# Performance work log

Measured on AMD Instinct MI355X. Metric: run time of the kernel, lower is better.

The kernel has to match this reference:

```python
import jax, jax.numpy as jnp
import numpy as np

KERNEL_BANDWIDTH = 0.3
STEP_SIZE = 0.5
NB_ITERATIONS = 4


def setup_inputs() -> dict:
    key = jax.random.key(0)
    # B x D x H x W pixel embeddings
    x_in = jax.random.normal(key, (2, 64, 96, 96), dtype=jnp.float32)
    return {"x_in": x_in}


def reference(x_in):
    B, D, H, W = x_in.shape
    N = H * W
    x0 = x_in.reshape(B, D, N)

    def body(x, _):
        # Gaussian-like kernel K[i,j] = exp(bw * <x_i, x_j>), symmetric NxN per batch
        K = jnp.exp(KERNEL_BANDWIDTH * jnp.einsum('bdn,bdm->bnm', x, x))  # (B,N,N)
        # torch: diag(K^T @ 1) then inverse of that diagonal == 1/column-sums
        colsum = jnp.sum(K, axis=1)  # (B,N)
        # x @ (K diag(1/colsum)): column-normalized weighted mean of embeddings
        xk = jnp.einsum('bdn,bnm->bdm', x, K) / colsum[:, None, :]
        x_new = STEP_SIZE * xk + (1.0 - STEP_SIZE) * x
        return x_new, x_new

    _, ys = jax.lax.scan(body, x0, None, length=NB_ITERATIONS)  # (I,B,D,N)
    allx = jnp.concatenate([x0[None], ys], axis=0)  # (I+1,B,D,N)
    # B x (I+1) x D x H x W
    return jnp.transpose(allx, (1, 0, 2, 3)).reshape(B, NB_ITERATIONS + 1, D, H, W)
```

## Files before the change

### kernel.cpp

```cpp
#include <hip/hip_runtime.h>
#include <hip/hip_bf16.h>

constexpr int B_    = 2;
constexpr int D_    = 64;
constexpr int N_    = 9216;
constexpr int ITERS = 4;

constexpr int MTQ     = 128;
constexpr int MBF     = N_ / MTQ;
constexpr int KS      = 4;
constexpr int KEYS_WG = N_ / KS;
constexpr int KTILES  = KEYS_WG / 128;
constexpr int NWG     = B_ * MBF * KS;
constexpr int PB      = 144;

constexpr float KBW  = 0.3f;
constexpr float STEP = 0.5f;
constexpr float C2   = 0.43280851226668905f;

using short8   = __attribute__((ext_vector_type(8))) short;
using float16v = __attribute__((ext_vector_type(16))) float;
typedef __attribute__((ext_vector_type(2))) __bf16 bf16x2;

__device__ __forceinline__ unsigned short f2bf(float f) {
  union { float f; unsigned u; } v; v.f = f;
  unsigned u = v.u;
  unsigned r = (u + 0x7fffu + ((u >> 16) & 1u)) >> 16;
  return (unsigned short)r;
}

#if __has_builtin(__builtin_amdgcn_cvt_pk_bf16_f32)
__device__ __forceinline__ unsigned pk2bf(float a, float b) {
  bf16x2 r = __builtin_amdgcn_cvt_pk_bf16_f32(a, b);
  union { bf16x2 h; unsigned u; } v; v.h = r; return v.u;
}
#else
__device__ __forceinline__ unsigned pk2bf(float a, float b) {
  return (unsigned)f2bf(a) | ((unsigned)f2bf(b) << 16);
}
#endif

__device__ __forceinline__ float csum2(unsigned u, float cs) {
#if __has_builtin(__builtin_amdgcn_fdot2_f32_bf16)
  union { unsigned x; bf16x2 h; } a, o;
  a.x = u; o.x = 0x3f803f80u;
  return __builtin_amdgcn_fdot2_f32_bf16(a.h, o.h, cs, false);
#else
  union { unsigned u; float f; } lo, hi;
  lo.u = u << 16; hi.u = u & 0xffff0000u;
  return cs + lo.f + hi.f;
#endif
}

__device__ __forceinline__ void dma16(const unsigned short* g,
                                      unsigned short* lds_base, int lane) {
#if __has_builtin(__builtin_amdgcn_global_load_lds)
  __builtin_amdgcn_global_load_lds(
      (const __attribute__((address_space(1))) unsigned int*)g,
      (__attribute__((address_space(3))) unsigned int*)lds_base, 16, 0, 0);
#else
  *(int4*)((char*)lds_base + lane * 16) = *(const int4*)g;
#endif
}

__global__ void prep_kernel(const float* __restrict__ xin, float* __restrict__ out,
                            unsigned short* __restrict__ XT,
                            unsigned short* __restrict__ Xbf)
{
  const int bx = blockIdx.x;
  const int nb = bx % PB, b = bx / PB;
  const int n0 = nb * 64;
  const int tid = threadIdx.x;
  __shared__ float tile[64 * 65];

  #pragma unroll
  for (int r = 0; r < 16; ++r) {
    int idx = r * 256 + tid;
    int d = idx >> 6, j = idx & 63;
    float v = xin[((size_t)b * 64 + d) * N_ + n0 + j];
    out[(((size_t)b * 5 + 0) * 64 + d) * N_ + n0 + j] = v;
    Xbf[((size_t)b * 64 + d) * N_ + n0 + j] = f2bf(v);
    tile[d * 65 + j] = v;
  }
  __syncthreads();
  #pragma unroll
  for (int r = 0; r < 16; ++r) {
    int idx = r * 256 + tid;
    int nl = idx >> 6, d = idx & 63;
    XT[((size_t)b * N_ + n0 + nl) * 64 + d] = f2bf(tile[d * 65 + nl]);
  }
}

__global__ void __launch_bounds__(256, 3) flash_kernel(
    const unsigned short* __restrict__ XT,
    const unsigned short* __restrict__ Xbf,
    float* __restrict__ pacc, float* __restrict__ pcs)
{
  const int bx   = blockIdx.x;
  const int ks   = bx & 3;
  const int mb   = (bx >> 2) % MBF;
  const int b    = bx / (MBF * KS);
  const int tid  = threadIdx.x;
  const int wave = tid >> 6, lane = tid & 63;
  const int c = lane & 31, h = lane >> 5;
  const int cp = (c & 0x13) | ((c & 4) << 1) | ((c & 8) >> 1);
  const int m0 = mb * MTQ;
  const int bpaddr = (lane ^ 32) << 2;

  const unsigned short* XTb = XT  + (size_t)b * N_ * 64;
  const unsigned short* Xb  = Xbf + (size_t)b * 64 * N_;

  __shared__ unsigned short sXT[128 * 64];
  __shared__ unsigned short sXB[64 * 128];

  short8 qf[4];
  #pragma unroll
  for (int k = 0; k < 4; ++k) {
    short8 raw = *(const short8*)(XTb +
        (size_t)(m0 + wave * 32 + c) * 64 + k * 16 + h * 8);
    unsigned o[4];
    const unsigned* rw = (const unsigned*)&raw;
    #pragma unroll
    for (int p4 = 0; p4 < 4; ++p4) {
      union { unsigned u; float f; } lo, hi;
      lo.u = rw[p4] << 16; hi.u = rw[p4] & 0xffff0000u;
      o[p4] = pk2bf(lo.f * C2, hi.f * C2);
    }
    qf[k] = *(const short8*)o;
  }

  float16v zv;
  #pragma unroll
  for (int p = 0; p < 16; ++p) zv[p] = 0.f;
  float16v acc[2];
  acc[0] = zv; acc[1] = zv;
  float cs = 0.f;

  const int xt_rr = lane >> 3, xt_sc = lane & 7;
  const int xb_rr = lane >> 4, xb_sc = lane & 15;

  int n0g = ks * KEYS_WG;
  for (int t = 0; t < KTILES; ++t, n0g += 128) {
    __syncthreads();
    #pragma unroll
    for (int ii = 0; ii < 4; ++ii) {
      int row = wave * 32 + ii * 8 + xt_rr;
      int gc  = xt_sc ^ (row & 7);
      dma16(XTb + (size_t)(n0g + row) * 64 + gc * 8,
            sXT + (wave * 32 + ii * 8) * 64, lane);
    }
    #pragma unroll
    for (int ii = 0; ii < 4; ++ii) {
      int row = wave * 16 + ii * 4 + xb_rr;
      int gc  = xb_sc ^ (row & 7);
      dma16(Xb + (size_t)row * N_ + n0g + gc * 8,
            sXB + (wave * 16 + ii * 4) * 128, lane);
    }
    __syncthreads();

    #pragma unroll
    for (int s = 0; s < 4; ++s) {
      short8 af[4];
      #pragma unroll
      for (int k = 0; k < 4; ++k)
        af[k] = *(const short8*)(sXT + (s * 32 + cp) * 64 +
                                 ((k * 2 + h) ^ (cp & 7)) * 8);

      float16v S = zv;
      #pragma unroll
      for (int k = 0; k < 4; ++k)
        S = __builtin_amdgcn_mfma_f32_32x32x16_bf16(af[k], qf[k], S, 0, 0, 0);

      unsigned q[8];
      #pragma unroll
      for (int g = 0; g < 8; ++g) {
        float w0 = __builtin_amdgcn_exp2f(S[2 * g]);
        float w1 = __builtin_amdgcn_exp2f(S[2 * g + 1]);
        unsigned u = pk2bf(w0, w1);
        q[g] = u;
        cs = csum2(u, cs);
      }

      union { unsigned d[4]; short8 s; } a20, a21;
      a20.d[0] = q[0]; a20.d[1] = q[1]; a20.d[2] = q[2]; a20.d[3] = q[3];
      a21.d[0] = q[4]; a21.d[1] = q[5]; a21.d[2] = q[6]; a21.d[3] = q[7];

      short8 b20[2], b21[2];
      #pragma unroll
      for (int dt = 0; dt < 2; ++dt) {
        b20[dt] = *(const short8*)(sXB + (dt * 32 + c) * 128 + ((4 * s + h)     ^ (c & 7)) * 8);
        b21[dt] = *(const short8*)(sXB + (dt * 32 + c) * 128 + ((4 * s + 2 + h) ^ (c & 7)) * 8);
      }
      #pragma unroll
      for (int dt = 0; dt < 2; ++dt)
        acc[dt] = __builtin_amdgcn_mfma_f32_32x32x16_bf16(a20.s, b20[dt], acc[dt], 0, 0, 0);
      #pragma unroll
      for (int dt = 0; dt < 2; ++dt)
        acc[dt] = __builtin_amdgcn_mfma_f32_32x32x16_bf16(a21.s, b21[dt], acc[dt], 0, 0, 0);
    }
  }

  union { float f; int i; } cu; cu.f = cs;
  cu.i = __builtin_amdgcn_ds_bpermute(bpaddr, cu.i);
  float cst = cs + cu.f;
  if (h == 0) pcs[(size_t)bx * 128 + wave * 32 + c] = cst;

  float* pw = pacc + (size_t)bx * (MTQ * 64);
  #pragma unroll
  for (int dt = 0; dt < 2; ++dt)
    #pragma unroll
    for (int p = 0; p < 16; ++p) {
      int m = wave * 32 + (p & 3) + 8 * (p >> 2) + 4 * h;
      pw[m * 64 + dt * 32 + c] = acc[dt][p];
    }
}

__global__ void combine_kernel(const float* __restrict__ pacc,
                               const float* __restrict__ pcs,
                               float* __restrict__ out,
                               unsigned short* __restrict__ XT,
                               unsigned short* __restrict__ Xbf, int t)
{
  const int bx = blockIdx.x;
  const int mb = bx % MBF, b = bx / MBF;
  const int m0 = mb * MTQ;
  const int tid = threadIdx.x;
  __shared__ float accs[128 * 65];
  __shared__ float cst[128];
  const int base = (b * MBF + mb) * KS;

  #pragma unroll
  for (int r = 0; r < 32; ++r) {
    int idx = r * 256 + tid;
    float s = 0.f;
    #pragma unroll
    for (int k = 0; k < KS; ++k) s += pacc[(size_t)(base + k) * 8192 + idx];
    accs[(idx >> 6) * 65 + (idx & 63)] = s;
  }
  if (tid < 128) {
    float cv = 0.f;
    #pragma unroll
    for (int k = 0; k < KS; ++k) cv += pcs[(size_t)(base + k) * 128 + tid];
    cst[tid] = cv;
  }
  __syncthreads();

  #pragma unroll
  for (int r = 0; r < 32; ++r) {
    int idx = r * 256 + tid;
    int m = idx & 127, d = idx >> 7;
    float a = accs[m * 65 + d];
    size_t obase = (((size_t)b * 5 + t) * 64 + d) * N_ + m0 + m;
    float xc = out[obase];
    float v = STEP * (a / cst[m]) + (1.f - STEP) * xc;
    out[obase + (size_t)64 * N_] = v;
    Xbf[((size_t)b * 64 + d) * N_ + m0 + m] = f2bf(v);
    accs[m * 65 + d] = v;
  }
  __syncthreads();

  #pragma unroll
  for (int r = 0; r < 32; ++r) {
    int idx = r * 256 + tid;
    int m = idx >> 6, d = idx & 63;
    XT[((size_t)b * N_ + m0 + m) * 64 + d] = f2bf(accs[m * 65 + d]);
  }
}

extern "C" void kernel_launch(void* const* d_in, const int* in_sizes, int n_in,
                              void* d_out, int out_size, void* d_ws, size_t ws_size,
                              hipStream_t stream)
{
  (void)in_sizes; (void)n_in; (void)out_size; (void)ws_size;
  const float* xin = (const float*)d_in[0];
  float* out = (float*)d_out;
  char* ws = (char*)d_ws;

  unsigned short* XT  = (unsigned short*)(ws);
  unsigned short* Xbf = (unsigned short*)(ws +  2359296);
  float*          pacc = (float*)(ws +  4718592);
  float*          pcs  = (float*)(ws + 23592960);

  prep_kernel<<<B_ * PB, 256, 0, stream>>>(xin, out, XT, Xbf);
  for (int t = 0; t < ITERS; ++t) {
    flash_kernel<<<NWG, 256, 0, stream>>>(XT, Xbf, pacc, pcs);
    combine_kernel<<<B_ * MBF, 256, 0, stream>>>(pacc, pcs, out, XT, Xbf, t);
  }
}
```

Baseline: 417.6 us.

## Double-buffer key tiles, split keys across waves, shrink query tile, widen combine grid

The flash kernel now double-buffers the shared-memory key tiles so the next tile's DMA overlaps the current tile's MFMA work, using one barrier per tile instead of two. Each wave takes a 32-key slice of every tile for a 64-query block, where before each wave owned 32 queries and walked all keys. Partial accumulators are then reduced across waves through shared memory. The query tile drops from 128 to 64, doubling the number of workgroups, and the combine kernel uses 32-row blocks with vectorized float4/float2 and packed bf16 accesses. The costs are twice the shared memory, a lower occupancy hint (2 instead of 3), and an extra cross-wave reduction step.

```diff
diff --git a/kernel.cpp b/kernel.cpp
--- a/kernel.cpp
+++ b/kernel.cpp
@@ -2,19 +2,18 @@
 #include <hip/hip_bf16.h>
 
 constexpr int B_    = 2;
-constexpr int D_    = 64;
 constexpr int N_    = 9216;
 constexpr int ITERS = 4;
 
-constexpr int MTQ     = 128;
+constexpr int MTQ     = 64;
 constexpr int MBF     = N_ / MTQ;
 constexpr int KS      = 4;
 constexpr int KEYS_WG = N_ / KS;
 constexpr int KTILES  = KEYS_WG / 128;
 constexpr int NWG     = B_ * MBF * KS;
 constexpr int PB      = 144;
-
-constexpr float KBW  = 0.3f;
+constexpr int CGRID   = B_ * (N_ / 32);
+
 constexpr float STEP = 0.5f;
 constexpr float C2   = 0.43280851226668905f;
 
@@ -91,7 +90,7 @@
   }
 }
 
-__global__ void __launch_bounds__(256, 3) flash_kernel(
+__global__ void __launch_bounds__(256, 2) flash_kernel(
     const unsigned short* __restrict__ XT,
     const unsigned short* __restrict__ Xbf,
     float* __restrict__ pacc, float* __restrict__ pcs)
@@ -101,118 +100,183 @@
   const int mb   = (bx >> 2) % MBF;
   const int b    = bx / (MBF * KS);
   const int tid  = threadIdx.x;
-  const int wave = tid >> 6, lane = tid & 63;
+  const int kw   = tid >> 6, lane = tid & 63;
   const int c = lane & 31, h = lane >> 5;
   const int cp = (c & 0x13) | ((c & 4) << 1) | ((c & 8) >> 1);
+  const int scp = (cp & 7) ^ ((cp & 8) >> 1);
   const int m0 = mb * MTQ;
-  const int bpaddr = (lane ^ 32) << 2;
 
   const unsigned short* XTb = XT  + (size_t)b * N_ * 64;
   const unsigned short* Xb  = Xbf + (size_t)b * 64 * N_;
 
-  __shared__ unsigned short sXT[128 * 64];
-  __shared__ unsigned short sXB[64 * 128];
-
-  short8 qf[4];
-  #pragma unroll
-  for (int k = 0; k < 4; ++k) {
-    short8 raw = *(const short8*)(XTb +
-        (size_t)(m0 + wave * 32 + c) * 64 + k * 16 + h * 8);
-    unsigned o[4];
-    const unsigned* rw = (const unsigned*)&raw;
-    #pragma unroll
-    for (int p4 = 0; p4 < 4; ++p4) {
-      union { unsigned u; float f; } lo, hi;
-      lo.u = rw[p4] << 16; hi.u = rw[p4] & 0xffff0000u;
-      o[p4] = pk2bf(lo.f * C2, hi.f * C2);
-    }
-    qf[k] = *(const short8*)o;
-  }
-
-  float16v zv;
-  #pragma unroll
-  for (int p = 0; p < 16; ++p) zv[p] = 0.f;
-  float16v acc[2];
-  acc[0] = zv; acc[1] = zv;
-  float cs = 0.f;
+  __shared__ __align__(16) unsigned short sXT[2][128 * 64];
+  __shared__ __align__(16) unsigned short sXB[2][64 * 128];
 
   const int xt_rr = lane >> 3, xt_sc = lane & 7;
   const int xb_rr = lane >> 4, xb_sc = lane & 15;
 
-  int n0g = ks * KEYS_WG;
-  for (int t = 0; t < KTILES; ++t, n0g += 128) {
-    __syncthreads();
+  auto stage = [&](int buf, int n0g) {
     #pragma unroll
     for (int ii = 0; ii < 4; ++ii) {
-      int row = wave * 32 + ii * 8 + xt_rr;
-      int gc  = xt_sc ^ (row & 7);
+      int row = kw * 32 + ii * 8 + xt_rr;
+      int gc  = xt_sc ^ ((row & 7) ^ ((row & 8) >> 1));
       dma16(XTb + (size_t)(n0g + row) * 64 + gc * 8,
-            sXT + (wave * 32 + ii * 8) * 64, lane);
+            &sXT[buf][(kw * 32 + ii * 8) * 64], lane);
     }
     #pragma unroll
     for (int ii = 0; ii < 4; ++ii) {
-      int row = wave * 16 + ii * 4 + xb_rr;
+      int row = kw * 16 + ii * 4 + xb_rr;
       int gc  = xb_sc ^ (row & 7);
       dma16(Xb + (size_t)row * N_ + n0g + gc * 8,
-            sXB + (wave * 16 + ii * 4) * 128, lane);
-    }
-    __syncthreads();
-
-    #pragma unroll
-    for (int s = 0; s < 4; ++s) {
-      short8 af[4];
+            &sXB[buf][(kw * 16 + ii * 4) * 128], lane);
+    }
+  };
+
+  const int n0g0 = ks * KEYS_WG;
+  stage(0, n0g0);
+
+  short8 qf[2][4];
+  #pragma unroll
+  for (int mt = 0; mt < 2; ++mt)
+    #pragma unroll
+    for (int k = 0; k < 4; ++k) {
+      short8 raw = *(const short8*)(XTb +
+          (size_t)(m0 + mt * 32 + c) * 64 + k * 16 + h * 8);
+      unsigned o[4];
+      const unsigned* rw = (const unsigned*)&raw;
+      #pragma unroll
+      for (int p4 = 0; p4 < 4; ++p4) {
+        union { unsigned u; float f; } lo, hi;
+        lo.u = rw[p4] << 16; hi.u = rw[p4] & 0xffff0000u;
+        o[p4] = pk2bf(lo.f * C2, hi.f * C2);
+      }
+      qf[mt][k] = *(const short8*)o;
+    }
+
+  float16v zv;
+  #pragma unroll
+  for (int p = 0; p < 16; ++p) zv[p] = 0.f;
+  float16v acc[2][2];
+  acc[0][0] = zv; acc[0][1] = zv; acc[1][0] = zv; acc[1][1] = zv;
+  float cs[2] = {0.f, 0.f};
+
+  __syncthreads();
+  int cur = 0;
+  const int s = kw;
+
+  for (int t = 0; t < KTILES; ++t) {
+    if (t + 1 < KTILES) stage(cur ^ 1, n0g0 + (t + 1) * 128);
+
+    const unsigned short* sT = &sXT[cur][0];
+    const unsigned short* sB = &sXB[cur][0];
+
+    short8 af[4];
+    #pragma unroll
+    for (int k = 0; k < 4; ++k)
+      af[k] = *(const short8*)(sT + (s * 32 + cp) * 64 +
+                               ((k * 2 + h) ^ scp) * 8);
+
+    short8 b20[2], b21[2];
+    #pragma unroll
+    for (int dt = 0; dt < 2; ++dt) {
+      b20[dt] = *(const short8*)(sB + (dt * 32 + c) * 128 + ((4 * s + h)     ^ (c & 7)) * 8);
+      b21[dt] = *(const short8*)(sB + (dt * 32 + c) * 128 + ((4 * s + 2 + h) ^ (c & 7)) * 8);
+    }
+
+    #pragma unroll
+    for (int mt = 0; mt < 2; ++mt) {
+      float16v S = zv;
       #pragma unroll
       for (int k = 0; k < 4; ++k)
-        af[k] = *(const short8*)(sXT + (s * 32 + cp) * 64 +
-                                 ((k * 2 + h) ^ (cp & 7)) * 8);
-
-      float16v S = zv;
-      #pragma unroll
-      for (int k = 0; k < 4; ++k)
-        S = __builtin_amdgcn_mfma_f32_32x32x16_bf16(af[k], qf[k], S, 0, 0, 0);
+        S = __builtin_amdgcn_mfma_f32_32x32x16_bf16(af[k], qf[mt][k], S, 0, 0, 0);
 
       unsigned q[8];
+      float csl = cs[mt];
       #pragma unroll
       for (int g = 0; g < 8; ++g) {
         float w0 = __builtin_amdgcn_exp2f(S[2 * g]);
         float w1 = __builtin_amdgcn_exp2f(S[2 * g + 1]);
         unsigned u = pk2bf(w0, w1);
         q[g] = u;
-        cs = csum2(u, cs);
+        csl = csum2(u, csl);
       }
-
-      union { unsigned d[4]; short8 s; } a20, a21;
+      cs[mt] = csl;
+
+      union { unsigned d[4]; short8 s8; } a20, a21;
       a20.d[0] = q[0]; a20.d[1] = q[1]; a20.d[2] = q[2]; a20.d[3] = q[3];
       a21.d[0] = q[4]; a21.d[1] = q[5]; a21.d[2] = q[6]; a21.d[3] = q[7];
 
-      short8 b20[2], b21[2];
-      #pragma unroll
-      for (int dt = 0; dt < 2; ++dt) {
-        b20[dt] = *(const short8*)(sXB + (dt * 32 + c) * 128 + ((4 * s + h)     ^ (c & 7)) * 8);
-        b21[dt] = *(const short8*)(sXB + (dt * 32 + c) * 128 + ((4 * s + 2 + h) ^ (c & 7)) * 8);
-      }
-      #pragma unroll
-      for (int dt = 0; dt < 2; ++dt)
-        acc[dt] = __builtin_amdgcn_mfma_f32_32x32x16_bf16(a20.s, b20[dt], acc[dt], 0, 0, 0);
-      #pragma unroll
-      for (int dt = 0; dt < 2; ++dt)
-        acc[dt] = __builtin_amdgcn_mfma_f32_32x32x16_bf16(a21.s, b21[dt], acc[dt], 0, 0, 0);
-    }
-  }
-
-  union { float f; int i; } cu; cu.f = cs;
-  cu.i = __builtin_amdgcn_ds_bpermute(bpaddr, cu.i);
-  float cst = cs + cu.f;
-  if (h == 0) pcs[(size_t)bx * 128 + wave * 32 + c] = cst;
-
-  float* pw = pacc + (size_t)bx * (MTQ * 64);
-  #pragma unroll
-  for (int dt = 0; dt < 2; ++dt)
-    #pragma unroll
-    for (int p = 0; p < 16; ++p) {
-      int m = wave * 32 + (p & 3) + 8 * (p >> 2) + 4 * h;
-      pw[m * 64 + dt * 32 + c] = acc[dt][p];
-    }
+      #pragma unroll
+      for (int dt = 0; dt < 2; ++dt)
+        acc[mt][dt] = __builtin_amdgcn_mfma_f32_32x32x16_bf16(a20.s8, b20[dt], acc[mt][dt], 0, 0, 0);
+      #pragma unroll
+      for (int dt = 0; dt < 2; ++dt)
+        acc[mt][dt] = __builtin_amdgcn_mfma_f32_32x32x16_bf16(a21.s8, b21[dt], acc[mt][dt], 0, 0, 0);
+    }
+
+    __syncthreads();
+    cur ^= 1;
+  }
+
+  float4* red = (float4*)&sXT[0][0];
+  float*  crd = (float*)&sXB[0][0];
+
+  auto dump = [&](int blk) {
+    #pragma unroll
+    for (int mt = 0; mt < 2; ++mt)
+      #pragma unroll
+      for (int dt = 0; dt < 2; ++dt)
+        #pragma unroll
+        for (int j = 0; j < 4; ++j) {
+          float4 v;
+          v.x = acc[mt][dt][4 * j + 0]; v.y = acc[mt][dt][4 * j + 1];
+          v.z = acc[mt][dt][4 * j + 2]; v.w = acc[mt][dt][4 * j + 3];
+          red[blk * 1024 + ((mt * 2 + dt) * 4 + j) * 64 + lane] = v;
+        }
+    crd[blk * 128 + lane]      = cs[0];
+    crd[blk * 128 + 64 + lane] = cs[1];
+  };
+  auto gather = [&](int blk) {
+    #pragma unroll
+    for (int mt = 0; mt < 2; ++mt)
+      #pragma unroll
+      for (int dt = 0; dt < 2; ++dt)
+        #pragma unroll
+        for (int j = 0; j < 4; ++j) {
+          float4 v = red[blk * 1024 + ((mt * 2 + dt) * 4 + j) * 64 + lane];
+          acc[mt][dt][4 * j + 0] += v.x; acc[mt][dt][4 * j + 1] += v.y;
+          acc[mt][dt][4 * j + 2] += v.z; acc[mt][dt][4 * j + 3] += v.w;
+        }
+    cs[0] += crd[blk * 128 + lane];
+    cs[1] += crd[blk * 128 + 64 + lane];
+  };
+
+  if (kw >= 2) dump(kw - 2);
+  __syncthreads();
+  if (kw < 2) gather(kw);
+  __syncthreads();
+  if (kw == 1) dump(0);
+  __syncthreads();
+  if (kw == 0) {
+    gather(0);
+    #pragma unroll
+    for (int mt = 0; mt < 2; ++mt) {
+      union { float f; int i; } cu; cu.f = cs[mt];
+      cu.i = __builtin_amdgcn_ds_bpermute((lane ^ 32) << 2, cu.i);
+      float cst = cs[mt] + cu.f;
+      if (h == 0) pcs[(size_t)bx * 64 + mt * 32 + c] = cst;
+    }
+    float* pw = pacc + (size_t)bx * (MTQ * 64);
+    #pragma unroll
+    for (int mt = 0; mt < 2; ++mt)
+      #pragma unroll
+      for (int dt = 0; dt < 2; ++dt)
+        #pragma unroll
+        for (int p = 0; p < 16; ++p) {
+          int m = mt * 32 + (p & 3) + 8 * (p >> 2) + 4 * h;
+          pw[m * 64 + dt * 32 + c] = acc[mt][dt][p];
+        }
+  }
 }
 
 __global__ void combine_kernel(const float* __restrict__ pacc,
@@ -221,49 +285,61 @@
                                unsigned short* __restrict__ XT,
                                unsigned short* __restrict__ Xbf, int t)
 {
-  const int bx = blockIdx.x;
-  const int mb = bx % MBF, b = bx / MBF;
-  const int m0 = mb * MTQ;
+  const int bx  = blockIdx.x;
+  const int mb2 = bx % 288, b = bx / 288;
+  const int m0  = mb2 * 32;
+  const int base = (b * MBF + (mb2 >> 1)) * KS;
+  const int poff = (mb2 & 1) * 2048;
+  const int coff = (mb2 & 1) * 32;
   const int tid = threadIdx.x;
-  __shared__ float accs[128 * 65];
-  __shared__ float cst[128];
-  const int base = (b * MBF + mb) * KS;
-
-  #pragma unroll
-  for (int r = 0; r < 32; ++r) {
+  __shared__ float accs[32 * 65];
+  __shared__ float cstl[32];
+
+  #pragma unroll
+  for (int r = 0; r < 2; ++r) {
+    int i4 = r * 256 + tid;
+    float4 s = make_float4(0.f, 0.f, 0.f, 0.f);
+    #pragma unroll
+    for (int k = 0; k < KS; ++k) {
+      const float4* p = (const float4*)(pacc + (size_t)(base + k) * 4096 + poff);
+      float4 v = p[i4];
+      s.x += v.x; s.y += v.y; s.z += v.z; s.w += v.w;
+    }
+    int m = i4 >> 4, d0 = (i4 & 15) * 4;
+    accs[m * 65 + d0 + 0] = s.x;
+    accs[m * 65 + d0 + 1] = s.y;
+    accs[m * 65 + d0 + 2] = s.z;
+    accs[m * 65 + d0 + 3] = s.w;
+  }
+  if (tid < 32) {
+    float cv = 0.f;
+    #pragma unroll
+    for (int k = 0; k < KS; ++k) cv += pcs[(size_t)(base + k) * 64 + coff + tid];
+    cstl[tid] = cv;
+  }
+  __syncthreads();
+
+  #pragma unroll
+  for (int r = 0; r < 4; ++r) {
     int idx = r * 256 + tid;
-    float s = 0.f;
-    #pragma unroll
-    for (int k = 0; k < KS; ++k) s += pacc[(size_t)(base + k) * 8192 + idx];
-    accs[(idx >> 6) * 65 + (idx & 63)] = s;
-  }
-  if (tid < 128) {
-    float cv = 0.f;
-    #pragma unroll
-    for (int k = 0; k < KS; ++k) cv += pcs[(size_t)(base + k) * 128 + tid];
-    cst[tid] = cv;
-  }
-  __syncthreads();
-
-  #pragma unroll
-  for (int r = 0; r < 32; ++r) {
+    int ml = (idx & 15) * 2, d = idx >> 4;
+    float a0 = accs[ml * 65 + d], a1 = accs[(ml + 1) * 65 + d];
+    size_t obase = (((size_t)b * 5 + t) * 64 + d) * N_ + m0 + ml;
+    float2 xc = *(const float2*)(out + obase);
+    float v0 = STEP * (a0 / cstl[ml])     + (1.f - STEP) * xc.x;
+    float v1 = STEP * (a1 / cstl[ml + 1]) + (1.f - STEP) * xc.y;
+    *(float2*)(out + obase + (size_t)64 * N_) = make_float2(v0, v1);
+    *(unsigned*)(Xbf + ((size_t)b * 64 + d) * N_ + m0 + ml) = pk2bf(v0, v1);
+    accs[ml * 65 + d] = v0; accs[(ml + 1) * 65 + d] = v1;
+  }
+  __syncthreads();
+
+  #pragma unroll
+  for (int r = 0; r < 4; ++r) {
     int idx = r * 256 + tid;
-    int m = idx & 127, d = idx >> 7;
-    float a = accs[m * 65 + d];
-    size_t obase = (((size_t)b * 5 + t) * 64 + d) * N_ + m0 + m;
-    float xc = out[obase];
-    float v = STEP * (a / cst[m]) + (1.f - STEP) * xc;
-    out[obase + (size_t)64 * N_] = v;
-    Xbf[((size_t)b * 64 + d) * N_ + m0 + m] = f2bf(v);
-    accs[m * 65 + d] = v;
-  }
-  __syncthreads();
-
-  #pragma unroll
-  for (int r = 0; r < 32; ++r) {
-    int idx = r * 256 + tid;
-    int m = idx >> 6, d = idx & 63;
-    XT[((size_t)b * N_ + m0 + m) * 64 + d] = f2bf(accs[m * 65 + d]);
+    int m = idx >> 5, d = (idx & 31) * 2;
+    *(unsigned*)(XT + ((size_t)b * N_ + m0 + m) * 64 + d)
+        = pk2bf(accs[m * 65 + d], accs[m * 65 + d + 1]);
   }
 }
 
@@ -284,6 +360,6 @@
   prep_kernel<<<B_ * PB, 256, 0, stream>>>(xin, out, XT, Xbf);
   for (int t = 0; t < ITERS; ++t) {
     flash_kernel<<<NWG, 256, 0, stream>>>(XT, Xbf, pacc, pcs);
-    combine_kernel<<<B_ * MBF, 256, 0, stream>>>(pacc, pcs, out, XT, Xbf, t);
-  }
-}
+    combine_kernel<<<CGRID, 256, 0, stream>>>(pacc, pcs, out, XT, Xbf, t);
+  }
+}
```

Result: slower. 434.1 us (+4.0%).

## Double-buffer key tiles in flash kernel and split combine into finer blocks

Applied to the files above, without the earlier changes.

The flash kernel now works on 64-key tiles held in two LDS buffers. The DMA for the next tile is issued before computing on the current one, and each iteration needs one barrier instead of two. This is meant to hide global-load latency behind the MFMA and exp work. The combine kernel moves from 144 blocks of 128 queries to 576 blocks of 32 queries, with vectorized float4/float2 loads and packed bf16 stores, to raise parallelism and memory efficiency. The cost is more loop iterations with smaller tiles, and any remaining barrier stalls.

```diff
diff --git a/kernel.cpp b/kernel.cpp
--- a/kernel.cpp
+++ b/kernel.cpp
@@ -2,7 +2,6 @@
 #include <hip/hip_bf16.h>
 
 constexpr int B_    = 2;
-constexpr int D_    = 64;
 constexpr int N_    = 9216;
 constexpr int ITERS = 4;
 
@@ -10,11 +9,12 @@
 constexpr int MBF     = N_ / MTQ;
 constexpr int KS      = 4;
 constexpr int KEYS_WG = N_ / KS;
-constexpr int KTILES  = KEYS_WG / 128;
+constexpr int KT      = 64;
+constexpr int KTILES  = KEYS_WG / KT;
 constexpr int NWG     = B_ * MBF * KS;
 constexpr int PB      = 144;
-
-constexpr float KBW  = 0.3f;
+constexpr int CGRID   = B_ * (N_ / 32);
+
 constexpr float STEP = 0.5f;
 constexpr float C2   = 0.43280851226668905f;
 
@@ -110,8 +110,30 @@
   const unsigned short* XTb = XT  + (size_t)b * N_ * 64;
   const unsigned short* Xb  = Xbf + (size_t)b * 64 * N_;
 
-  __shared__ unsigned short sXT[128 * 64];
-  __shared__ unsigned short sXB[64 * 128];
+  __shared__ __align__(16) unsigned short sXT[2][KT * 64];
+  __shared__ __align__(16) unsigned short sXB[2][64 * KT];
+
+  const int rr = lane >> 3, sc = lane & 7;
+  const int gc = sc ^ rr;
+
+  const int n0g0 = ks * KEYS_WG;
+
+  const unsigned short* xtp  = XTb + (size_t)(n0g0 + wave * 16 + rr) * 64 + gc * 8;
+  const unsigned short* xbp0 = Xb  + (size_t)(wave * 16 + rr) * N_ + n0g0 + gc * 8;
+  const unsigned short* xbp1 = xbp0 + (size_t)8 * N_;
+
+  auto stage = [&](int buf, const unsigned short* xt_,
+                   const unsigned short* xb0_, const unsigned short* xb1_) {
+    unsigned short* lt = &sXT[buf][wave * 16 * 64];
+    unsigned short* lb = &sXB[buf][wave * 16 * 64];
+    dma16(xt_,       lt,       lane);
+    dma16(xt_ + 512, lt + 512, lane);
+    dma16(xb0_,      lb,       lane);
+    dma16(xb1_,      lb + 512, lane);
+  };
+
+  stage(0, xtp, xbp0, xbp1);
+  xtp += KT * 64; xbp0 += KT; xbp1 += KT;
 
   short8 qf[4];
   #pragma unroll
@@ -129,6 +151,19 @@
     qf[k] = *(const short8*)o;
   }
 
+  const int e = cp & 7;
+  const unsigned short* afb[4];
+  #pragma unroll
+  for (int k = 0; k < 4; ++k)
+    afb[k] = &sXT[0][cp * 64 + ((2 * k + h) ^ e) * 8];
+  const int ec = c & 7;
+  const unsigned short* bfb0[2], * bfb1[2];
+  #pragma unroll
+  for (int s = 0; s < 2; ++s) {
+    bfb0[s] = &sXB[0][c * 64 + ((4 * s +     h) ^ ec) * 8];
+    bfb1[s] = &sXB[0][c * 64 + ((4 * s + 2 + h) ^ ec) * 8];
+  }
+
   float16v zv;
   #pragma unroll
   for (int p = 0; p < 16; ++p) zv[p] = 0.f;
@@ -136,35 +171,22 @@
   acc[0] = zv; acc[1] = zv;
   float cs = 0.f;
 
-  const int xt_rr = lane >> 3, xt_sc = lane & 7;
-  const int xb_rr = lane >> 4, xb_sc = lane & 15;
-
-  int n0g = ks * KEYS_WG;
-  for (int t = 0; t < KTILES; ++t, n0g += 128) {
-    __syncthreads();
-    #pragma unroll
-    for (int ii = 0; ii < 4; ++ii) {
-      int row = wave * 32 + ii * 8 + xt_rr;
-      int gc  = xt_sc ^ (row & 7);
-      dma16(XTb + (size_t)(n0g + row) * 64 + gc * 8,
-            sXT + (wave * 32 + ii * 8) * 64, lane);
-    }
-    #pragma unroll
-    for (int ii = 0; ii < 4; ++ii) {
-      int row = wave * 16 + ii * 4 + xb_rr;
-      int gc  = xb_sc ^ (row & 7);
-      dma16(Xb + (size_t)row * N_ + n0g + gc * 8,
-            sXB + (wave * 16 + ii * 4) * 128, lane);
-    }
-    __syncthreads();
-
-    #pragma unroll
-    for (int s = 0; s < 4; ++s) {
+  __syncthreads();
+
+  #pragma unroll 2
+  for (int t = 0; t < KTILES; ++t) {
+    const int buf = t & 1;
+    if (t + 1 < KTILES) {
+      stage(buf ^ 1, xtp, xbp0, xbp1);
+      xtp += KT * 64; xbp0 += KT; xbp1 += KT;
+    }
+
+    #pragma unroll
+    for (int s = 0; s < 2; ++s) {
       short8 af[4];
       #pragma unroll
       for (int k = 0; k < 4; ++k)
-        af[k] = *(const short8*)(sXT + (s * 32 + cp) * 64 +
-                                 ((k * 2 + h) ^ (cp & 7)) * 8);
+        af[k] = *(const short8*)(afb[k] + buf * 4096 + s * 2048);
 
       float16v S = zv;
       #pragma unroll
@@ -181,23 +203,25 @@
         cs = csum2(u, cs);
       }
 
-      union { unsigned d[4]; short8 s; } a20, a21;
+      union { unsigned d[4]; short8 s8; } a20, a21;
       a20.d[0] = q[0]; a20.d[1] = q[1]; a20.d[2] = q[2]; a20.d[3] = q[3];
       a21.d[0] = q[4]; a21.d[1] = q[5]; a21.d[2] = q[6]; a21.d[3] = q[7];
 
       short8 b20[2], b21[2];
       #pragma unroll
       for (int dt = 0; dt < 2; ++dt) {
-        b20[dt] = *(const short8*)(sXB + (dt * 32 + c) * 128 + ((4 * s + h)     ^ (c & 7)) * 8);
-        b21[dt] = *(const short8*)(sXB + (dt * 32 + c) * 128 + ((4 * s + 2 + h) ^ (c & 7)) * 8);
+        b20[dt] = *(const short8*)(bfb0[s] + buf * 4096 + dt * 2048);
+        b21[dt] = *(const short8*)(bfb1[s] + buf * 4096 + dt * 2048);
       }
       #pragma unroll
       for (int dt = 0; dt < 2; ++dt)
-        acc[dt] = __builtin_amdgcn_mfma_f32_32x32x16_bf16(a20.s, b20[dt], acc[dt], 0, 0, 0);
+        acc[dt] = __builtin_amdgcn_mfma_f32_32x32x16_bf16(a20.s8, b20[dt], acc[dt], 0, 0, 0);
       #pragma unroll
       for (int dt = 0; dt < 2; ++dt)
-        acc[dt] = __builtin_amdgcn_mfma_f32_32x32x16_bf16(a21.s, b21[dt], acc[dt], 0, 0, 0);
-    }
+        acc[dt] = __builtin_amdgcn_mfma_f32_32x32x16_bf16(a21.s8, b21[dt], acc[dt], 0, 0, 0);
+    }
+
+    __syncthreads();
   }
 
   union { float f; int i; } cu; cu.f = cs;
@@ -221,49 +245,61 @@
                                unsigned short* __restrict__ XT,
                                unsigned short* __restrict__ Xbf, int t)
 {
-  const int bx = blockIdx.x;
-  const int mb = bx % MBF, b = bx / MBF;
-  const int m0 = mb * MTQ;
+  const int bx  = blockIdx.x;
+  const int q32 = bx % 288, b = bx / 288;
+  const int m0  = q32 * 32;
+  const int base = (b * MBF + (q32 >> 2)) * KS;
+  const int poff = (q32 & 3) * 2048;
+  const int coff = (q32 & 3) * 32;
   const int tid = threadIdx.x;
-  __shared__ float accs[128 * 65];
-  __shared__ float cst[128];
-  const int base = (b * MBF + mb) * KS;
-
-  #pragma unroll
-  for (int r = 0; r < 32; ++r) {
+  __shared__ float accs[32 * 65];
+  __shared__ float cstl[32];
+
+  #pragma unroll
+  for (int r = 0; r < 2; ++r) {
+    int i4 = r * 256 + tid;
+    float4 s = make_float4(0.f, 0.f, 0.f, 0.f);
+    #pragma unroll
+    for (int k = 0; k < KS; ++k) {
+      const float4* p = (const float4*)(pacc + (size_t)(base + k) * 8192 + poff);
+      float4 v = p[i4];
+      s.x += v.x; s.y += v.y; s.z += v.z; s.w += v.w;
+    }
+    int m = i4 >> 4, d0 = (i4 & 15) * 4;
+    accs[m * 65 + d0 + 0] = s.x;
+    accs[m * 65 + d0 + 1] = s.y;
+    accs[m * 65 + d0 + 2] = s.z;
+    accs[m * 65 + d0 + 3] = s.w;
+  }
+  if (tid < 32) {
+    float cv = 0.f;
+    #pragma unroll
+    for (int k = 0; k < KS; ++k) cv += pcs[(size_t)(base + k) * 128 + coff + tid];
+    cstl[tid] = cv;
+  }
+  __syncthreads();
+
+  #pragma unroll
+  for (int r = 0; r < 4; ++r) {
     int idx = r * 256 + tid;
-    float s = 0.f;
-    #pragma unroll
-    for (int k = 0; k < KS; ++k) s += pacc[(size_t)(base + k) * 8192 + idx];
-    accs[(idx >> 6) * 65 + (idx & 63)] = s;
-  }
-  if (tid < 128) {
-    float cv = 0.f;
-    #pragma unroll
-    for (int k = 0; k < KS; ++k) cv += pcs[(size_t)(base + k) * 128 + tid];
-    cst[tid] = cv;
+    int ml = (idx & 15) * 2, d = idx >> 4;
+    float a0 = accs[ml * 65 + d], a1 = accs[(ml + 1) * 65 + d];
+    size_t obase = (((size_t)b * 5 + t) * 64 + d) * N_ + m0 + ml;
+    float2 xc = *(const float2*)(out + obase);
+    float v0 = STEP * (a0 / cstl[ml])     + (1.f - STEP) * xc.x;
+    float v1 = STEP * (a1 / cstl[ml + 1]) + (1.f - STEP) * xc.y;
+    *(float2*)(out + obase + (size_t)64 * N_) = make_float2(v0, v1);
+    *(unsigned*)(Xbf + ((size_t)b * 64 + d) * N_ + m0 + ml) = pk2bf(v0, v1);
+    accs[ml * 65 + d] = v0; accs[(ml + 1) * 65 + d] = v1;
   }
   __syncthreads();
 
   #pragma unroll
-  for (int r = 0; r < 32; ++r) {
+  for (int r = 0; r < 4; ++r) {
     int idx = r * 256 + tid;
-    int m = idx & 127, d = idx >> 7;
-    float a = accs[m * 65 + d];
-    size_t obase = (((size_t)b * 5 + t) * 64 + d) * N_ + m0 + m;
-    float xc = out[obase];
-    float v = STEP * (a / cst[m]) + (1.f - STEP) * xc;
-    out[obase + (size_t)64 * N_] = v;
-    Xbf[((size_t)b * 64 + d) * N_ + m0 + m] = f2bf(v);
-    accs[m * 65 + d] = v;
-  }
-  __syncthreads();
-
-  #pragma unroll
-  for (int r = 0; r < 32; ++r) {
-    int idx = r * 256 + tid;
-    int m = idx >> 6, d = idx & 63;
-    XT[((size_t)b * N_ + m0 + m) * 64 + d] = f2bf(accs[m * 65 + d]);
+    int m = idx >> 5, d = (idx & 31) * 2;
+    *(unsigned*)(XT + ((size_t)b * N_ + m0 + m) * 64 + d)
+        = pk2bf(accs[m * 65 + d], accs[m * 65 + d + 1]);
   }
 }
 
@@ -284,6 +320,6 @@
   prep_kernel<<<B_ * PB, 256, 0, stream>>>(xin, out, XT, Xbf);
   for (int t = 0; t < ITERS; ++t) {
     flash_kernel<<<NWG, 256, 0, stream>>>(XT, Xbf, pacc, pcs);
-    combine_kernel<<<B_ * MBF, 256, 0, stream>>>(pacc, pcs, out, XT, Xbf, t);
-  }
-}
+    combine_kernel<<<CGRID, 256, 0, stream>>>(pacc, pcs, out, XT, Xbf, t);
+  }
+}
```

Result: faster. 373.8 us (-10.5%).
